# Kernel tuning notes

Hardware: AMD Instinct MI355X
Metric: run time of the kernel (lower is better)

## Reference

```python
import jax, jax.numpy as jnp
import numpy as np

D_INPUT = 900; D_MODEL = 900; D_STATE = 16; D_CONV = 4
D_INNER = 1800; DT_RANK = 57  # ceil(900/16)
B_SZ = 2; L = 900


def build_pe():
    # Faithful to the (non-standard) loop in PositionalEncoding.__init__
    pos = np.arange(D_INPUT, dtype=np.float64)[:, None]
    pe = np.zeros((D_INPUT, D_MODEL), dtype=np.float64)
    i_even = np.arange(0, D_MODEL, 2, dtype=np.float64)
    i_odd = np.arange(1, D_MODEL, 2, dtype=np.float64)
    pe[:, 0::2] = np.sin(pos / 10000.0 ** (2.0 * i_even / D_MODEL))
    pe[:, 1::2] = np.cos(pos / 10000.0 ** (2.0 * (i_odd + 1.0) / D_MODEL))
    return jnp.asarray(pe, jnp.float32)


def setup_inputs() -> dict:
    key = jax.random.key(0)
    ks = jax.random.split(key, 8)
    s = 0.02
    inp = jax.random.normal(ks[0], (B_SZ, L, D_INPUT), jnp.float32)
    W_emb = jax.random.normal(ks[1], (D_MODEL, D_INPUT), jnp.float32) * s
    b_emb = jnp.zeros((D_MODEL,), jnp.float32)
    norm_w = jnp.ones((D_MODEL,), jnp.float32)
    W_in = jax.random.normal(ks[2], (2 * D_INNER, D_MODEL), jnp.float32) * s
    conv_w = jax.random.normal(ks[3], (D_INNER, 1, D_CONV), jnp.float32) * s
    conv_b = jnp.zeros((D_INNER,), jnp.float32)
    W_xp = jax.random.normal(ks[4], (DT_RANK + 2 * D_STATE, D_INNER), jnp.float32) * s
    W_dt = jax.random.normal(ks[5], (D_INNER, DT_RANK), jnp.float32) * s
    b_dt = jnp.zeros((D_INNER,), jnp.float32)
    A_log = jnp.log(jnp.broadcast_to(jnp.arange(1, D_STATE + 1, dtype=jnp.float32), (D_INNER, D_STATE)))
    D = jnp.ones((D_INNER,), jnp.float32)
    W_out = jax.random.normal(ks[6], (D_MODEL, D_INNER), jnp.float32) * s
    normf_w = jnp.ones((D_MODEL,), jnp.float32)
    pe = build_pe()
    return dict(inp=inp, W_emb=W_emb, b_emb=b_emb, norm_w=norm_w, W_in=W_in,
                conv_w=conv_w, conv_b=conv_b, W_xp=W_xp, W_dt=W_dt, b_dt=b_dt,
                A_log=A_log, D=D, W_out=W_out, normf_w=normf_w, pe=pe)


def rmsnorm(x, w, eps=1e-5):
    return x * jax.lax.rsqrt(jnp.mean(x * x, axis=-1, keepdims=True) + eps) * w


def causal_dwconv(x, w, b):
    # x: (b, l, d_in); torch Conv1d(groups=d_in, padding=k-1) then [:, :, :l] == causal left-pad
    xc = jnp.transpose(x, (0, 2, 1))  # (b, d_in, l)
    y = jax.lax.conv_general_dilated(xc, w, window_strides=(1,),
                                     padding=[(D_CONV - 1, 0)],
                                     dimension_numbers=('NCH', 'OIH', 'NCH'),
                                     feature_group_count=D_INNER)
    return jnp.transpose(y + b[None, :, None], (0, 2, 1))


def selective_scan(u, delta, A, Bm, Cm, Dv):
    # u, delta: (b, l, d_in); A: (d_in, n); Bm, Cm: (b, l, n); Dv: (d_in,)
    dA = jnp.exp(jnp.einsum('bld,dn->bldn', delta, A))
    dBu = jnp.einsum('bld,bln,bld->bldn', delta, Bm, u)

    def step(h, xs):
        dA_i, dBu_i, C_i = xs
        h = dA_i * h + dBu_i                      # (b, d_in, n)
        y = jnp.einsum('bdn,bn->bd', h, C_i)
        return h, y

    h0 = jnp.zeros((u.shape[0], D_INNER, D_STATE), u.dtype)
    _, ys = jax.lax.scan(step, h0, (jnp.moveaxis(dA, 1, 0), jnp.moveaxis(dBu, 1, 0), jnp.moveaxis(Cm, 1, 0)))
    return jnp.moveaxis(ys, 0, 1) + u * Dv


def mamba_block(x, W_in, conv_w, conv_b, W_xp, W_dt, b_dt, A_log, Dv, W_out):
    xr = x @ W_in.T                               # (b, l, 2*d_inner)
    xm, res = xr[..., :D_INNER], xr[..., D_INNER:]
    xb = xm[..., ::-1]  # NOTE: original flips dim 2 == channel dim, not sequence
    xm = jax.nn.silu(causal_dwconv(xm, conv_w, conv_b))
    xb = jax.nn.silu(causal_dwconv(xb, conv_w, conv_b))

    def ssm(u):
        A = -jnp.exp(A_log)
        xd = u @ W_xp.T                           # (b, l, dt_rank + 2n)
        delta = jax.nn.softplus(xd[..., :DT_RANK] @ W_dt.T + b_dt)
        Bm = xd[..., DT_RANK:DT_RANK + D_STATE]
        Cm = xd[..., DT_RANK + D_STATE:]
        return selective_scan(u, delta, A, Bm, Cm, Dv)

    y = ssm(xm)
    yb = ssm(xb)[..., ::-1]  # flip back over channels, as in original
    g = jax.nn.silu(res)
    return (y * g + yb * g) @ W_out.T


def reference(inp, W_emb, b_emb, norm_w, W_in, conv_w, conv_b, W_xp, W_dt, b_dt, A_log, D, W_out, normf_w, pe):
    x = inp @ W_emb.T + b_emb                     # embedding Linear
    x = x * jnp.sqrt(jnp.float32(D_MODEL)) + pe[None, :x.shape[1]]
    x = mamba_block(rmsnorm(x, norm_w), W_in, conv_w, conv_b, W_xp, W_dt, b_dt, A_log, D, W_out) + x
    x = rmsnorm(x, normf_w)
    logits = x.reshape(x.shape[0], -1)
    return (logits,)
```

## Files before the change

### kernel.cpp

```cpp
#include <hip/hip_runtime.h>
#include <math.h>

typedef unsigned short ushortT;
typedef short short8 __attribute__((ext_vector_type(8)));
typedef float f32x4 __attribute__((ext_vector_type(4)));

#define D_STATE 16
#define D_INNER 1800
#define DT_RANK 57
#define SEQ_L 900
#define MROWS 1800
#define MP 1920
#define KP_DM 960
#define KP_DI 1856
#define KP_DT 64
#define NCHUNK 45
#define CLEN 20

__device__ __forceinline__ ushortT f2bf(float f) {
    unsigned u = __float_as_uint(f);
    unsigned r = (u + 0x7FFFu + ((u >> 16) & 1u)) >> 16;
    return (ushortT)r;
}
__device__ __forceinline__ float bf2f(ushortT h) {
    return __uint_as_float((unsigned)h << 16);
}
__device__ __forceinline__ float silu_f(float x) { return x / (1.f + __expf(-x)); }
__device__ __forceinline__ float softplus_f(float x) {
    return fmaxf(x, 0.f) + __logf(1.f + __expf(-fabsf(x)));
}

__device__ __forceinline__ void gload_lds16(const ushortT* g, ushortT* l) {
    __builtin_amdgcn_global_load_lds((const __attribute__((address_space(1))) unsigned int*)g,
                                     (__attribute__((address_space(3))) unsigned int*)l,
                                     16, 0, 0);
}

__global__ __launch_bounds__(256)
void cvt_all_k(const float* __restrict__ s0, ushortT* __restrict__ d0,
               const float* __restrict__ s1, ushortT* __restrict__ d1,
               const float* __restrict__ s2, ushortT* __restrict__ d2,
               const float* __restrict__ s3, ushortT* __restrict__ d3,
               const float* __restrict__ s4, ushortT* __restrict__ d4,
               const float* __restrict__ s5, ushortT* __restrict__ d5)
{
    const float* src; ushortT* dst; int M, K, Mp, Kp;
    switch (blockIdx.y) {
      case 0: src=s0; dst=d0; M=1800; K=900;  Mp=1920; Kp=960;  break;
      case 1: src=s1; dst=d1; M=900;  K=900;  Mp=1024; Kp=960;  break;
      case 2: src=s2; dst=d2; M=3600; K=900;  Mp=3712; Kp=960;  break;
      case 3: src=s3; dst=d3; M=89;   K=1800; Mp=128;  Kp=1856; break;
      case 4: src=s4; dst=d4; M=1800; K=57;   Mp=1920; Kp=64;   break;
      default:src=s5; dst=d5; M=900;  K=1800; Mp=1024; Kp=1856; break;
    }
    int t = blockIdx.x * 256 + threadIdx.x;
    int K4 = Kp >> 2;
    if (t >= Mp * K4) return;
    int r = t / K4, c4 = (t - r * K4) * 4;
    ushortT o[4];
#pragma unroll
    for (int e = 0; e < 4; ++e) {
        int c = c4 + e;
        float v = (r < M && c < K) ? src[(size_t)r * K + c] : 0.f;
        o[e] = f2bf(v);
    }
    uint2 pk;
    pk.x = (unsigned)o[0] | ((unsigned)o[1] << 16);
    pk.y = (unsigned)o[2] | ((unsigned)o[3] << 16);
    *(uint2*)(dst + (size_t)r * Kp + c4) = pk;
}

__global__ __launch_bounds__(256)
void gemm_mfma_k(const ushortT* __restrict__ A0, const ushortT* __restrict__ A1, int lda,
                 const ushortT* __restrict__ Bw, int ldb, int nkTotal, int split,
                 float* __restrict__ C0, float* __restrict__ C1, int ldc, size_t cstride,
                 ushortT* __restrict__ X0, ushortT* __restrict__ X1, int ldx, size_t xstride,
                 int M, int N, const float* __restrict__ bias, int mode)
{
    __shared__ ushortT As[2][128 * 64];
    __shared__ ushortT Bs[2][128 * 64];

    int gx = gridDim.x, gy = gridDim.y;
    int nwg = gx * gy * gridDim.z;
    int orig = (blockIdx.z * gy + blockIdx.y) * gx + blockIdx.x;
    int q8 = nwg >> 3, r8 = nwg & 7;
    int xcd = orig & 7, i8 = orig >> 3;
    int wg = (xcd < r8 ? xcd * (q8 + 1) : r8 * (q8 + 1) + (xcd - r8) * q8) + i8;
    int bx = wg % gx; int tmp = wg / gx; int by = tmp % gy; int bz = tmp / gy;

    int dir = bz / split, s = bz % split;
    int per = (nkTotal + split - 1) / split;
    int kt0 = s * per;
    int kcnt = nkTotal - kt0; if (kcnt > per) kcnt = per;
    int ktEnd = kt0 + kcnt;

    const ushortT* A = dir ? A1 : A0;
    float* C = (dir ? C1 : C0);
    ushortT* Xo = (dir ? X1 : X0);
    if (C)  C  += (size_t)s * cstride;
    if (Xo) Xo += (size_t)s * xstride;

    int tid = threadIdx.x;
    int lane = tid & 63, wave = tid >> 6;
    int wr = wave >> 1, wc = wave & 1;
    int m0 = by * 128, n0 = bx * 128;

    int csw = ((((tid >> 3) & 7) ^ (tid & 7)) << 3);
    auto stage = [&](int sb, int kt) {
#pragma unroll
        for (int r = 0; r < 4; ++r) {
            int idx = r * 256 + tid;
            int row = idx >> 3;
            gload_lds16(A + (size_t)(m0 + row) * lda + kt * 64 + csw, &As[sb][idx * 8]);
        }
#pragma unroll
        for (int r = 0; r < 4; ++r) {
            int idx = r * 256 + tid;
            int row = idx >> 3;
            gload_lds16(Bw + (size_t)(n0 + row) * ldb + kt * 64 + csw, &Bs[sb][idx * 8]);
        }
    };

    f32x4 acc[4][4] = {};
    int rmask = (lane & 7) << 3;

    stage(0, kt0);
    for (int t = kt0; t < ktEnd; ++t) {
        int cur = (t - kt0) & 1;
        if (t + 1 < ktEnd) {
            stage(cur ^ 1, t + 1);
            asm volatile("s_waitcnt vmcnt(8)" ::: "memory");
        } else {
            asm volatile("s_waitcnt vmcnt(0)" ::: "memory");
        }
        __builtin_amdgcn_s_barrier();
        __builtin_amdgcn_sched_barrier(0);
#pragma unroll
        for (int ks = 0; ks < 2; ++ks) {
            short8 av[4], bv[4];
            int kcol = (ks * 32 + (lane >> 4) * 8) ^ rmask;
#pragma unroll
            for (int i = 0; i < 4; ++i)
                av[i] = *(const short8*)(&As[cur][(wr * 64 + i * 16 + (lane & 15)) * 64 + kcol]);
#pragma unroll
            for (int j = 0; j < 4; ++j)
                bv[j] = *(const short8*)(&Bs[cur][(wc * 64 + j * 16 + (lane & 15)) * 64 + kcol]);
#pragma unroll
            for (int i = 0; i < 4; ++i)
#pragma unroll
                for (int j = 0; j < 4; ++j)
                    acc[i][j] = __builtin_amdgcn_mfma_f32_16x16x32_bf16(bv[j], av[i], acc[i][j], 0, 0, 0);
        }
        __builtin_amdgcn_sched_barrier(0);
        __builtin_amdgcn_s_barrier();
        __builtin_amdgcn_sched_barrier(0);
    }

#pragma unroll
    for (int i = 0; i < 4; ++i) {
        int m = m0 + wr * 64 + i * 16 + (lane & 15);
        if (m >= M) continue;
#pragma unroll
        for (int j = 0; j < 4; ++j) {
            int nb = n0 + wc * 64 + j * 16 + (lane >> 4) * 4;
            if (nb >= N) continue;
            f32x4 v = acc[i][j];
            if (mode == 5) {
#pragma unroll
                for (int e = 0; e < 4; ++e)
                    v[e] = softplus_f(v[e] + bias[nb + e]);
            }
            if (mode == 1 || mode == 5) {
                unsigned lo, hi;
                asm("v_cvt_pk_bf16_f32 %0, %1, %2" : "=v"(lo) : "v"(v[0]), "v"(v[1]));
                asm("v_cvt_pk_bf16_f32 %0, %1, %2" : "=v"(hi) : "v"(v[2]), "v"(v[3]));
                uint2 pk; pk.x = lo; pk.y = hi;
                *(uint2*)(Xo + (size_t)m * ldx + nb) = pk;
            } else {
                *(f32x4*)(C + (size_t)m * ldc + nb) = v;
            }
        }
    }
}

__global__ __launch_bounds__(256)
void rmsnorm_emb_k(const ushortT* __restrict__ P, size_t pstride,
                   const float* __restrict__ b_emb, const float* __restrict__ pe,
                   const float* __restrict__ norm_w,
                   float* __restrict__ XS, ushortT* __restrict__ XN, int ldxn)
{
    int row = blockIdx.x;
    int l = (row >= SEQ_L) ? row - SEQ_L : row;
    float vv[4];
    float ssum = 0.f;
#pragma unroll
    for (int k = 0; k < 4; ++k) {
        int c = threadIdx.x + k * 256;
        if (c < 900) {
            size_t i = (size_t)row * 900 + c;
            float a = bf2f(P[i]) + bf2f(P[i + pstride]) + bf2f(P[i + 2 * pstride]) + bf2f(P[i + 3 * pstride]);
            float v = 30.f * (a + b_emb[c]) + pe[(size_t)l * 900 + c];
            vv[k] = v;
            ssum += v * v;
        } else vv[k] = 0.f;
    }
#pragma unroll
    for (int off = 32; off; off >>= 1) ssum += __shfl_down(ssum, off, 64);
    __shared__ float red[4];
    int wv = threadIdx.x >> 6;
    if ((threadIdx.x & 63) == 0) red[wv] = ssum;
    __syncthreads();
    float tot = red[0] + red[1] + red[2] + red[3];
    float scale = rsqrtf(tot / 900.f + 1e-5f);
#pragma unroll
    for (int k = 0; k < 4; ++k) {
        int c = threadIdx.x + k * 256;
        if (c < 900) {
            XS[(size_t)row * 900 + c] = vv[k];
            XN[(size_t)row * ldxn + c] = f2bf(vv[k] * scale * norm_w[c]);
        }
    }
}

__global__ __launch_bounds__(256)
void rmsnorm_final_k(const ushortT* __restrict__ ZP, size_t zstride,
                     const float* __restrict__ XS, const float* __restrict__ w,
                     float* __restrict__ out)
{
    int row = blockIdx.x;
    float vv[4];
    float ssum = 0.f;
#pragma unroll
    for (int k = 0; k < 4; ++k) {
        int c = threadIdx.x + k * 256;
        if (c < 900) {
            size_t i = (size_t)row * 900 + c;
            float v = bf2f(ZP[i]) + bf2f(ZP[i + zstride]) + bf2f(ZP[i + 2 * zstride]) + bf2f(ZP[i + 3 * zstride]) + XS[i];
            vv[k] = v;
            ssum += v * v;
        } else vv[k] = 0.f;
    }
#pragma unroll
    for (int off = 32; off; off >>= 1) ssum += __shfl_down(ssum, off, 64);
    __shared__ float red[4];
    int wv = threadIdx.x >> 6;
    if ((threadIdx.x & 63) == 0) red[wv] = ssum;
    __syncthreads();
    float tot = red[0] + red[1] + red[2] + red[3];
    float scale = rsqrtf(tot / 900.f + 1e-5f);
#pragma unroll
    for (int k = 0; k < 4; ++k) {
        int c = threadIdx.x + k * 256;
        if (c < 900) out[(size_t)row * 900 + c] = vv[k] * scale * w[c];
    }
}

__global__ __launch_bounds__(256)
void conv_silu_k(const ushortT* __restrict__ xr0, const ushortT* __restrict__ xr1,
                 const float* __restrict__ w, const float* __restrict__ cb,
                 ushortT* __restrict__ xmc, ushortT* __restrict__ xbc,
                 ushortT* __restrict__ gout)
{
    int t = blockIdx.x * 256 + threadIdx.x;
    if (t >= MROWS * (D_INNER / 2)) return;
    int d0 = (t % (D_INNER / 2)) * 2;
    int row = t / (D_INNER / 2);
    int l = row % SEQ_L;
    float w0[4], w1[4];
#pragma unroll
    for (int k = 0; k < 4; ++k) { w0[k] = w[d0 * 4 + k]; w1[k] = w[d0 * 4 + 4 + k]; }
    int rdp = 1798 - d0;
    float sf0 = cb[d0], sf1 = cb[d0 + 1];
    float sb0 = sf0, sb1 = sf1;
#pragma unroll
    for (int k = 0; k < 4; ++k) {
        int ll = l - 3 + k;
        if (ll < 0) continue;
        size_t ro = (size_t)(row - l + ll) * 3600;
        unsigned f0 = *(const unsigned*)(xr0 + ro + d0);
        unsigned f1 = *(const unsigned*)(xr1 + ro + d0);
        float a0 = bf2f((ushortT)f0) + bf2f((ushortT)f1);
        float a1 = bf2f((ushortT)(f0 >> 16)) + bf2f((ushortT)(f1 >> 16));
        sf0 = fmaf(w0[k], a0, sf0);
        sf1 = fmaf(w1[k], a1, sf1);
        unsigned r0 = *(const unsigned*)(xr0 + ro + rdp);
        unsigned r1 = *(const unsigned*)(xr1 + ro + rdp);
        float b0 = bf2f((ushortT)(r0 >> 16)) + bf2f((ushortT)(r1 >> 16));
        float b1 = bf2f((ushortT)r0) + bf2f((ushortT)r1);
        sb0 = fmaf(w0[k], b0, sb0);
        sb1 = fmaf(w1[k], b1, sb1);
    }
    unsigned om = (unsigned)f2bf(silu_f(sf0)) | ((unsigned)f2bf(silu_f(sf1)) << 16);
    unsigned ob = (unsigned)f2bf(silu_f(sb0)) | ((unsigned)f2bf(silu_f(sb1)) << 16);
    *(unsigned*)(xmc + (size_t)row * KP_DI + d0) = om;
    *(unsigned*)(xbc + (size_t)row * KP_DI + d0) = ob;
    size_t rr = (size_t)row * 3600 + D_INNER + d0;
    unsigned g0 = *(const unsigned*)(xr0 + rr);
    unsigned g1 = *(const unsigned*)(xr1 + rr);
    float ga = silu_f(bf2f((ushortT)g0) + bf2f((ushortT)g1));
    float gb = silu_f(bf2f((ushortT)(g0 >> 16)) + bf2f((ushortT)(g1 >> 16)));
    *(unsigned*)(gout + (size_t)row * D_INNER + d0) = (unsigned)f2bf(ga) | ((unsigned)f2bf(gb) << 16);
}

__global__ __launch_bounds__(256)
void xp_reduce_k(const float* __restrict__ XPp, size_t pstride,
                 float* __restrict__ XDC, ushortT* __restrict__ XDMb, ushortT* __restrict__ XDBb)
{
    int t = blockIdx.x * 256 + threadIdx.x;
    if (t >= 2 * MROWS * 96) return;
    int dir = t / (MROWS * 96);
    int rem = t - dir * (MROWS * 96);
    int row = rem / 96, c = rem - row * 96;
    const float* basep = XPp + (size_t)dir * 8 * pstride + (size_t)row * 96 + c;
    float s = 0.f;
#pragma unroll
    for (int p = 0; p < 8; ++p) s += basep[p * pstride];
    ushortT* xdb = dir ? XDBb : XDMb;
    if (c < DT_RANK)           xdb[(size_t)row * KP_DT + c] = f2bf(s);
    else if (c < KP_DT)        xdb[(size_t)row * KP_DT + c] = 0;
    if (c >= DT_RANK && c < DT_RANK + 2 * D_STATE)
        XDC[((size_t)dir * MROWS + row) * 32 + (c - DT_RANK)] = s;
}

__global__ __launch_bounds__(256)
void scan_l1_k(const ushortT* __restrict__ DMb, const ushortT* __restrict__ DBb,
               const ushortT* __restrict__ Um, const ushortT* __restrict__ Ub,
               const float* __restrict__ XDC, const float* __restrict__ A_log,
               ushortT* __restrict__ HL, float* __restrict__ SD)
{
    int d = blockIdx.x * 256 + threadIdx.x;
    if (d >= D_INNER) return;
    int c = blockIdx.y, zz = blockIdx.z;
    int b = zz >> 1, dir = zz & 1;
    const ushortT* DL = dir ? DBb : DMb;
    const ushortT* U = dir ? Ub : Um;
    const float* XD = XDC + (size_t)dir * MROWS * 32;
    float Aa[D_STATE];
#pragma unroll
    for (int n = 0; n < D_STATE; ++n) Aa[n] = -__expf(A_log[d * D_STATE + n]);
    float h[D_STATE] = {};
    float S = 0.f;
    int l0 = c * CLEN;
    for (int i = 0; i < CLEN; ++i) {
        size_t rowi = (size_t)b * SEQ_L + l0 + i;
        float delta = bf2f(DL[rowi * D_INNER + d]);
        float u = bf2f(U[rowi * KP_DI + d]);
        const float* bc = XD + rowi * 32;
        float du = delta * u;
        S += delta;
#pragma unroll
        for (int n = 0; n < D_STATE; ++n)
            h[n] = fmaf(__expf(delta * Aa[n]), h[n], du * bc[n]);
    }
    ushortT* hp = HL + ((size_t)(zz * NCHUNK + c) * D_INNER + d) * D_STATE;
    unsigned pk[8];
#pragma unroll
    for (int q = 0; q < 8; ++q)
        asm("v_cvt_pk_bf16_f32 %0, %1, %2" : "=v"(pk[q]) : "v"(h[2*q]), "v"(h[2*q+1]));
    uint4 lo4; lo4.x = pk[0]; lo4.y = pk[1]; lo4.z = pk[2]; lo4.w = pk[3];
    uint4 hi4; hi4.x = pk[4]; hi4.y = pk[5]; hi4.z = pk[6]; hi4.w = pk[7];
    *(uint4*)(hp) = lo4;
    *(uint4*)(hp + 8) = hi4;
    SD[(size_t)(zz * NCHUNK + c) * D_INNER + d] = S;
}

__global__ __launch_bounds__(256)
void scan_l2_k(ushortT* __restrict__ HL, const float* __restrict__ SD,
               const float* __restrict__ A_log)
{
    int t = blockIdx.x * 256 + threadIdx.x;
    if (t >= 4 * D_INNER * D_STATE) return;
    int n = t & 15;
    int d = (t >> 4) % D_INNER;
    int zz = t / (D_INNER * D_STATE);
    float Aa = -__expf(A_log[d * D_STATE + n]);
    float h0 = 0.f;
    for (int c = 0; c < NCHUNK; ++c) {
        size_t ih = ((size_t)(zz * NCHUNK + c) * D_INNER + d) * D_STATE + n;
        float hl = bf2f(HL[ih]);
        float T = __expf(Aa * SD[(size_t)(zz * NCHUNK + c) * D_INNER + d]);
        HL[ih] = f2bf(h0);
        h0 = fmaf(T, h0, hl);
    }
}

__global__ __launch_bounds__(256)
void scan3_gate_k(const ushortT* __restrict__ DMb, const ushortT* __restrict__ DBb,
                  const ushortT* __restrict__ Um, const ushortT* __restrict__ Ub,
                  const float* __restrict__ XDC, const float* __restrict__ A_log,
                  const float* __restrict__ Dv, const ushortT* __restrict__ HL,
                  const ushortT* __restrict__ G, ushortT* __restrict__ YC)
{
    int d = blockIdx.x * 256 + threadIdx.x;
    if (d >= D_INNER) return;
    int c = blockIdx.y, b = blockIdx.z;
    int rd = D_INNER - 1 - d;
    float Aa0[D_STATE], Aa1[D_STATE], h0[D_STATE], h1[D_STATE];
#pragma unroll
    for (int n = 0; n < D_STATE; ++n) Aa0[n] = -__expf(A_log[d * D_STATE + n]);
#pragma unroll
    for (int n = 0; n < D_STATE; ++n) Aa1[n] = -__expf(A_log[rd * D_STATE + n]);
    const ushortT* hp0 = HL + ((size_t)((b * 2) * NCHUNK + c) * D_INNER + d) * D_STATE;
    const ushortT* hp1 = HL + ((size_t)((b * 2 + 1) * NCHUNK + c) * D_INNER + rd) * D_STATE;
    {
        uint4 a0 = *(const uint4*)(hp0);
        uint4 a1 = *(const uint4*)(hp0 + 8);
        unsigned ww[8] = {a0.x, a0.y, a0.z, a0.w, a1.x, a1.y, a1.z, a1.w};
#pragma unroll
        for (int q = 0; q < 8; ++q) {
            h0[2*q]   = bf2f((ushortT)ww[q]);
            h0[2*q+1] = bf2f((ushortT)(ww[q] >> 16));
        }
        uint4 b0 = *(const uint4*)(hp1);
        uint4 b1 = *(const uint4*)(hp1 + 8);
        unsigned vv[8] = {b0.x, b0.y, b0.z, b0.w, b1.x, b1.y, b1.z, b1.w};
#pragma unroll
        for (int q = 0; q < 8; ++q) {
            h1[2*q]   = bf2f((ushortT)vv[q]);
            h1[2*q+1] = bf2f((ushortT)(vv[q] >> 16));
        }
    }
    float Dd0 = Dv[d], Dd1 = Dv[rd];
    const float* XD0 = XDC;
    const float* XD1 = XDC + (size_t)MROWS * 32;
    int l0 = c * CLEN;
    for (int i = 0; i < CLEN; ++i) {
        size_t rowi = (size_t)b * SEQ_L + l0 + i;
        float delta0 = bf2f(DMb[rowi * D_INNER + d]);
        float u0 = bf2f(Um[rowi * KP_DI + d]);
        const float* bc0 = XD0 + rowi * 32;
        float du0 = delta0 * u0;
        float acc0 = u0 * Dd0;
#pragma unroll
        for (int n = 0; n < D_STATE; ++n) {
            h0[n] = fmaf(__expf(delta0 * Aa0[n]), h0[n], du0 * bc0[n]);
            acc0 = fmaf(h0[n], bc0[D_STATE + n], acc0);
        }
        float delta1 = bf2f(DBb[rowi * D_INNER + rd]);
        float u1 = bf2f(Ub[rowi * KP_DI + rd]);
        const float* bc1 = XD1 + rowi * 32;
        float du1 = delta1 * u1;
        float acc1 = u1 * Dd1;
#pragma unroll
        for (int n = 0; n < D_STATE; ++n) {
            h1[n] = fmaf(__expf(delta1 * Aa1[n]), h1[n], du1 * bc1[n]);
            acc1 = fmaf(h1[n], bc1[D_STATE + n], acc1);
        }
        float g = bf2f(G[rowi * D_INNER + d]);
        YC[rowi * KP_DI + d] = f2bf((acc0 + acc1) * g);
    }
}

extern "C" void kernel_launch(void* const* d_in, const int* in_sizes, int n_in,
                              void* d_out, int out_size, void* d_ws, size_t ws_size,
                              hipStream_t stream)
{
    const float* inp    = (const float*)d_in[0];
    const float* W_emb  = (const float*)d_in[1];
    const float* b_emb  = (const float*)d_in[2];
    const float* norm_w = (const float*)d_in[3];
    const float* W_in   = (const float*)d_in[4];
    const float* conv_w = (const float*)d_in[5];
    const float* conv_b = (const float*)d_in[6];
    const float* W_xp   = (const float*)d_in[7];
    const float* W_dt   = (const float*)d_in[8];
    const float* b_dt   = (const float*)d_in[9];
    const float* A_log  = (const float*)d_in[10];
    const float* Dv     = (const float*)d_in[11];
    const float* W_out  = (const float*)d_in[12];
    const float* normf_w= (const float*)d_in[13];
    const float* pe     = (const float*)d_in[14];

    char* base = (char*)d_ws;
    size_t off = 0;
    auto alloc = [&](size_t bytes) { char* p = base + off; off += (bytes + 255) & ~(size_t)255; return p; };

    float*   XS      = (float*)alloc(6480000);
    char*    arena1  = alloc(22032000);
    float*   XPp     = (float*)arena1;
    ushortT* HL      = (ushortT*)arena1;
    float*   SD      = (float*)(arena1 + 10368000);
    ushortT* inp_bf  = (ushortT*)alloc(3686400);
    ushortT* XN_bf   = (ushortT*)alloc(3686400);
    ushortT* Wemb_bf = (ushortT*)alloc(1966080);
    ushortT* Win_bf  = (ushortT*)alloc(7127040);
    ushortT* Wxp_bf  = (ushortT*)alloc(475136);
    ushortT* Wdt_bf  = (ushortT*)alloc(245760);
    ushortT* Wout_bf = (ushortT*)alloc(3801088);
    ushortT* XBC_bf  = (ushortT*)alloc(7127040);
    char*    arena2  = alloc(25920000);
    ushortT* Pemb    = (ushortT*)arena2;
    ushortT* XR0     = (ushortT*)arena2;
    ushortT* XR1     = XR0 + (size_t)MROWS * 3600;
    ushortT* DMb     = (ushortT*)arena2;
    ushortT* DBb     = DMb + (size_t)MROWS * D_INNER;
    ushortT* ZP      = (ushortT*)arena2;
    ushortT* G_bf    = (ushortT*)alloc(6480000);

    float*   XDC     = (float*)Wemb_bf;
    ushortT* XDM_bf  = (ushortT*)((char*)Wemb_bf + 460800);
    ushortT* XDB_bf  = (ushortT*)((char*)Wemb_bf + 706560);
    ushortT* XMC_bf  = Win_bf;
    ushortT* YC_bf   = inp_bf;

    dim3 blk(256);
    auto cdiv = [](int a, int b) { return (a + b - 1) / b; };
    const size_t PSTR  = 1620000;
    const size_t XPSTR = 172800;
    const size_t XRSTR = (size_t)MROWS * 3600;

    hipLaunchKernelGGL(cvt_all_k, dim3(3480, 6), blk, 0, stream,
                       inp, inp_bf, W_emb, Wemb_bf, W_in, Win_bf,
                       W_xp, Wxp_bf, W_dt, Wdt_bf, W_out, Wout_bf);
    hipLaunchKernelGGL(gemm_mfma_k, dim3(8, 15, 4), blk, 0, stream,
                       inp_bf, inp_bf, KP_DM, Wemb_bf, KP_DM, KP_DM/64, 4,
                       (float*)nullptr, (float*)nullptr, 0, (size_t)0,
                       Pemb, Pemb, 900, PSTR,
                       MROWS, 900, (const float*)nullptr, 1);
    hipLaunchKernelGGL(rmsnorm_emb_k, dim3(MROWS), blk, 0, stream,
                       Pemb, PSTR, b_emb, pe, norm_w, XS, XN_bf, KP_DM);
    hipLaunchKernelGGL(gemm_mfma_k, dim3(29, 15, 2), blk, 0, stream,
                       XN_bf, XN_bf, KP_DM, Win_bf, KP_DM, KP_DM/64, 2,
                       (float*)nullptr, (float*)nullptr, 0, (size_t)0,
                       XR0, XR0, 3600, XRSTR,
                       MROWS, 3600, (const float*)nullptr, 1);
    hipLaunchKernelGGL(conv_silu_k, dim3(cdiv(MROWS * (D_INNER/2), 256)), blk, 0, stream,
                       XR0, XR1, conv_w, conv_b, XMC_bf, XBC_bf, G_bf);
    hipLaunchKernelGGL(gemm_mfma_k, dim3(1, 15, 16), blk, 0, stream,
                       XMC_bf, XBC_bf, KP_DI, Wxp_bf, KP_DI, KP_DI/64, 8,
                       XPp, XPp + 8 * XPSTR, 96, XPSTR,
                       (ushortT*)nullptr, (ushortT*)nullptr, 0, (size_t)0,
                       MROWS, 96, (const float*)nullptr, 0);
    hipLaunchKernelGGL(xp_reduce_k, dim3(cdiv(2 * MROWS * 96, 256)), blk, 0, stream,
                       XPp, XPSTR, XDC, XDM_bf, XDB_bf);
    hipLaunchKernelGGL(gemm_mfma_k, dim3(15, 15, 2), blk, 0, stream,
                       XDM_bf, XDB_bf, KP_DT, Wdt_bf, KP_DT, 1, 1,
                       (float*)nullptr, (float*)nullptr, 0, (size_t)0,
                       DMb, DBb, D_INNER, (size_t)0,
                       MROWS, D_INNER, b_dt, 5);
    hipLaunchKernelGGL(scan_l1_k, dim3(cdiv(D_INNER, 256), NCHUNK, 4), blk, 0, stream,
                       DMb, DBb, XMC_bf, XBC_bf, XDC, A_log, HL, SD);
    hipLaunchKernelGGL(scan_l2_k, dim3(cdiv(4 * D_INNER * D_STATE, 256)), blk, 0, stream, HL, SD, A_log);
    hipLaunchKernelGGL(scan3_gate_k, dim3(cdiv(D_INNER, 256), NCHUNK, 2), blk, 0, stream,
                       DMb, DBb, XMC_bf, XBC_bf, XDC, A_log, Dv, HL, G_bf, YC_bf);
    hipLaunchKernelGGL(gemm_mfma_k, dim3(8, 15, 4), blk, 0, stream,
                       YC_bf, YC_bf, KP_DI, Wout_bf, KP_DI, KP_DI/64, 4,
                       (float*)nullptr, (float*)nullptr, 0, (size_t)0,
                       ZP, ZP, 900, PSTR,
                       MROWS, 900, (const float*)nullptr, 1);
    hipLaunchKernelGGL(rmsnorm_final_k, dim3(MROWS), blk, 0, stream,
                       ZP, PSTR, XS, normf_w, (float*)d_out);
}
```

Measured before the change: 284.7 us.

## Drop split-K on in_proj GEMM, fuse gate SiLU into epilogue, widen conv/cvt vectors

Measured after the change: 276.7 us. 1.03x faster.

```diff
diff --git a/kernel.cpp b/kernel.cpp
--- a/kernel.cpp
+++ b/kernel.cpp
@@ -54,20 +54,19 @@
       default:src=s5; dst=d5; M=900;  K=1800; Mp=1024; Kp=1856; break;
     }
     int t = blockIdx.x * 256 + threadIdx.x;
-    int K4 = Kp >> 2;
-    if (t >= Mp * K4) return;
-    int r = t / K4, c4 = (t - r * K4) * 4;
-    ushortT o[4];
-#pragma unroll
-    for (int e = 0; e < 4; ++e) {
-        int c = c4 + e;
-        float v = (r < M && c < K) ? src[(size_t)r * K + c] : 0.f;
-        o[e] = f2bf(v);
-    }
-    uint2 pk;
-    pk.x = (unsigned)o[0] | ((unsigned)o[1] << 16);
-    pk.y = (unsigned)o[2] | ((unsigned)o[3] << 16);
-    *(uint2*)(dst + (size_t)r * Kp + c4) = pk;
+    int K8 = Kp >> 3;
+    if (t >= Mp * K8) return;
+    int r = t / K8, c8 = (t - r * K8) * 8;
+    unsigned pk[4];
+#pragma unroll
+    for (int q = 0; q < 4; ++q) {
+        int ca = c8 + 2 * q, cb = ca + 1;
+        float va = (r < M && ca < K) ? src[(size_t)r * K + ca] : 0.f;
+        float vb = (r < M && cb < K) ? src[(size_t)r * K + cb] : 0.f;
+        pk[q] = (unsigned)f2bf(va) | ((unsigned)f2bf(vb) << 16);
+    }
+    uint4 o; o.x = pk[0]; o.y = pk[1]; o.z = pk[2]; o.w = pk[3];
+    *(uint4*)(dst + (size_t)r * Kp + c8) = o;
 }
 
 __global__ __launch_bounds__(256)
@@ -97,7 +96,7 @@
     const ushortT* A = dir ? A1 : A0;
     float* C = (dir ? C1 : C0);
     ushortT* Xo = (dir ? X1 : X0);
-    if (C)  C  += (size_t)s * cstride;
+    if (C && mode != 6)  C  += (size_t)s * cstride;
     if (Xo) Xo += (size_t)s * xstride;
 
     int tid = threadIdx.x;
@@ -170,7 +169,24 @@
                 for (int e = 0; e < 4; ++e)
                     v[e] = softplus_f(v[e] + bias[nb + e]);
             }
-            if (mode == 1 || mode == 5) {
+            if (mode == 6) {
+                if (nb < D_INNER) {
+                    unsigned lo, hi;
+                    asm("v_cvt_pk_bf16_f32 %0, %1, %2" : "=v"(lo) : "v"(v[0]), "v"(v[1]));
+                    asm("v_cvt_pk_bf16_f32 %0, %1, %2" : "=v"(hi) : "v"(v[2]), "v"(v[3]));
+                    uint2 pk; pk.x = lo; pk.y = hi;
+                    *(uint2*)(Xo + (size_t)m * ldx + nb) = pk;
+                } else {
+                    ushortT* G = (ushortT*)C;
+#pragma unroll
+                    for (int e = 0; e < 4; ++e) v[e] = silu_f(v[e]);
+                    unsigned lo, hi;
+                    asm("v_cvt_pk_bf16_f32 %0, %1, %2" : "=v"(lo) : "v"(v[0]), "v"(v[1]));
+                    asm("v_cvt_pk_bf16_f32 %0, %1, %2" : "=v"(hi) : "v"(v[2]), "v"(v[3]));
+                    uint2 pk; pk.x = lo; pk.y = hi;
+                    *(uint2*)(G + (size_t)m * D_INNER + (nb - D_INNER)) = pk;
+                }
+            } else if (mode == 1 || mode == 5) {
                 unsigned lo, hi;
                 asm("v_cvt_pk_bf16_f32 %0, %1, %2" : "=v"(lo) : "v"(v[0]), "v"(v[1]));
                 asm("v_cvt_pk_bf16_f32 %0, %1, %2" : "=v"(hi) : "v"(v[2]), "v"(v[3]));
@@ -256,50 +272,51 @@
 }
 
 __global__ __launch_bounds__(256)
-void conv_silu_k(const ushortT* __restrict__ xr0, const ushortT* __restrict__ xr1,
+void conv_silu_k(const ushortT* __restrict__ xr,
                  const float* __restrict__ w, const float* __restrict__ cb,
-                 ushortT* __restrict__ xmc, ushortT* __restrict__ xbc,
-                 ushortT* __restrict__ gout)
+                 ushortT* __restrict__ xmc, ushortT* __restrict__ xbc)
 {
     int t = blockIdx.x * 256 + threadIdx.x;
-    if (t >= MROWS * (D_INNER / 2)) return;
-    int d0 = (t % (D_INNER / 2)) * 2;
-    int row = t / (D_INNER / 2);
+    if (t >= MROWS * (D_INNER / 4)) return;
+    int d0 = (t % (D_INNER / 4)) * 4;
+    int row = t / (D_INNER / 4);
     int l = row % SEQ_L;
-    float w0[4], w1[4];
-#pragma unroll
-    for (int k = 0; k < 4; ++k) { w0[k] = w[d0 * 4 + k]; w1[k] = w[d0 * 4 + 4 + k]; }
-    int rdp = 1798 - d0;
-    float sf0 = cb[d0], sf1 = cb[d0 + 1];
-    float sb0 = sf0, sb1 = sf1;
+    float wv[4][4], sf[4], sb[4];
+#pragma unroll
+    for (int ch = 0; ch < 4; ++ch) {
+        f32x4 wl = *(const f32x4*)(w + (d0 + ch) * 4);
+        wv[ch][0] = wl[0]; wv[ch][1] = wl[1]; wv[ch][2] = wl[2]; wv[ch][3] = wl[3];
+        float b = cb[d0 + ch];
+        sf[ch] = b; sb[ch] = b;
+    }
+    int rdp = 1796 - d0;
 #pragma unroll
     for (int k = 0; k < 4; ++k) {
         int ll = l - 3 + k;
         if (ll < 0) continue;
-        size_t ro = (size_t)(row - l + ll) * 3600;
-        unsigned f0 = *(const unsigned*)(xr0 + ro + d0);
-        unsigned f1 = *(const unsigned*)(xr1 + ro + d0);
-        float a0 = bf2f((ushortT)f0) + bf2f((ushortT)f1);
-        float a1 = bf2f((ushortT)(f0 >> 16)) + bf2f((ushortT)(f1 >> 16));
-        sf0 = fmaf(w0[k], a0, sf0);
-        sf1 = fmaf(w1[k], a1, sf1);
-        unsigned r0 = *(const unsigned*)(xr0 + ro + rdp);
-        unsigned r1 = *(const unsigned*)(xr1 + ro + rdp);
-        float b0 = bf2f((ushortT)(r0 >> 16)) + bf2f((ushortT)(r1 >> 16));
-        float b1 = bf2f((ushortT)r0) + bf2f((ushortT)r1);
-        sb0 = fmaf(w0[k], b0, sb0);
-        sb1 = fmaf(w1[k], b1, sb1);
-    }
-    unsigned om = (unsigned)f2bf(silu_f(sf0)) | ((unsigned)f2bf(silu_f(sf1)) << 16);
-    unsigned ob = (unsigned)f2bf(silu_f(sb0)) | ((unsigned)f2bf(silu_f(sb1)) << 16);
-    *(unsigned*)(xmc + (size_t)row * KP_DI + d0) = om;
-    *(unsigned*)(xbc + (size_t)row * KP_DI + d0) = ob;
-    size_t rr = (size_t)row * 3600 + D_INNER + d0;
-    unsigned g0 = *(const unsigned*)(xr0 + rr);
-    unsigned g1 = *(const unsigned*)(xr1 + rr);
-    float ga = silu_f(bf2f((ushortT)g0) + bf2f((ushortT)g1));
-    float gb = silu_f(bf2f((ushortT)(g0 >> 16)) + bf2f((ushortT)(g1 >> 16)));
-    *(unsigned*)(gout + (size_t)row * D_INNER + d0) = (unsigned)f2bf(ga) | ((unsigned)f2bf(gb) << 16);
+        const ushortT* rp = xr + (size_t)(row - l + ll) * D_INNER;
+        uint2 f = *(const uint2*)(rp + d0);
+        float a0 = bf2f((ushortT)f.x), a1 = bf2f((ushortT)(f.x >> 16));
+        float a2 = bf2f((ushortT)f.y), a3 = bf2f((ushortT)(f.y >> 16));
+        sf[0] = fmaf(wv[0][k], a0, sf[0]);
+        sf[1] = fmaf(wv[1][k], a1, sf[1]);
+        sf[2] = fmaf(wv[2][k], a2, sf[2]);
+        sf[3] = fmaf(wv[3][k], a3, sf[3]);
+        uint2 rv = *(const uint2*)(rp + rdp);
+        float b0 = bf2f((ushortT)rv.x), b1 = bf2f((ushortT)(rv.x >> 16));
+        float b2 = bf2f((ushortT)rv.y), b3 = bf2f((ushortT)(rv.y >> 16));
+        sb[0] = fmaf(wv[0][k], b3, sb[0]);
+        sb[1] = fmaf(wv[1][k], b2, sb[1]);
+        sb[2] = fmaf(wv[2][k], b1, sb[2]);
+        sb[3] = fmaf(wv[3][k], b0, sb[3]);
+    }
+    uint2 om, ob;
+    om.x = (unsigned)f2bf(silu_f(sf[0])) | ((unsigned)f2bf(silu_f(sf[1])) << 16);
+    om.y = (unsigned)f2bf(silu_f(sf[2])) | ((unsigned)f2bf(silu_f(sf[3])) << 16);
+    ob.x = (unsigned)f2bf(silu_f(sb[0])) | ((unsigned)f2bf(silu_f(sb[1])) << 16);
+    ob.y = (unsigned)f2bf(silu_f(sb[2])) | ((unsigned)f2bf(silu_f(sb[3])) << 16);
+    *(uint2*)(xmc + (size_t)row * KP_DI + d0) = om;
+    *(uint2*)(xbc + (size_t)row * KP_DI + d0) = ob;
 }
 
 __global__ __launch_bounds__(256)
@@ -490,8 +507,7 @@
     ushortT* XBC_bf  = (ushortT*)alloc(7127040);
     char*    arena2  = alloc(25920000);
     ushortT* Pemb    = (ushortT*)arena2;
-    ushortT* XR0     = (ushortT*)arena2;
-    ushortT* XR1     = XR0 + (size_t)MROWS * 3600;
+    ushortT* XR      = (ushortT*)arena2;
     ushortT* DMb     = (ushortT*)arena2;
     ushortT* DBb     = DMb + (size_t)MROWS * D_INNER;
     ushortT* ZP      = (ushortT*)arena2;
@@ -507,9 +523,8 @@
     auto cdiv = [](int a, int b) { return (a + b - 1) / b; };
     const size_t PSTR  = 1620000;
     const size_t XPSTR = 172800;
-    const size_t XRSTR = (size_t)MROWS * 3600;
-
-    hipLaunchKernelGGL(cvt_all_k, dim3(3480, 6), blk, 0, stream,
+
+    hipLaunchKernelGGL(cvt_all_k, dim3(1740, 6), blk, 0, stream,
                        inp, inp_bf, W_emb, Wemb_bf, W_in, Win_bf,
                        W_xp, Wxp_bf, W_dt, Wdt_bf, W_out, Wout_bf);
     hipLaunchKernelGGL(gemm_mfma_k, dim3(8, 15, 4), blk, 0, stream,
@@ -519,13 +534,13 @@
                        MROWS, 900, (const float*)nullptr, 1);
     hipLaunchKernelGGL(rmsnorm_emb_k, dim3(MROWS), blk, 0, stream,
                        Pemb, PSTR, b_emb, pe, norm_w, XS, XN_bf, KP_DM);
-    hipLaunchKernelGGL(gemm_mfma_k, dim3(29, 15, 2), blk, 0, stream,
-                       XN_bf, XN_bf, KP_DM, Win_bf, KP_DM, KP_DM/64, 2,
-                       (float*)nullptr, (float*)nullptr, 0, (size_t)0,
-                       XR0, XR0, 3600, XRSTR,
-                       MROWS, 3600, (const float*)nullptr, 1);
-    hipLaunchKernelGGL(conv_silu_k, dim3(cdiv(MROWS * (D_INNER/2), 256)), blk, 0, stream,
-                       XR0, XR1, conv_w, conv_b, XMC_bf, XBC_bf, G_bf);
+    hipLaunchKernelGGL(gemm_mfma_k, dim3(29, 15, 1), blk, 0, stream,
+                       XN_bf, XN_bf, KP_DM, Win_bf, KP_DM, KP_DM/64, 1,
+                       (float*)G_bf, (float*)G_bf, 0, (size_t)0,
+                       XR, XR, D_INNER, (size_t)0,
+                       MROWS, 3600, (const float*)nullptr, 6);
+    hipLaunchKernelGGL(conv_silu_k, dim3(cdiv(MROWS * (D_INNER/4), 256)), blk, 0, stream,
+                       XR, conv_w, conv_b, XMC_bf, XBC_bf);
     hipLaunchKernelGGL(gemm_mfma_k, dim3(1, 15, 16), blk, 0, stream,
                        XMC_bf, XBC_bf, KP_DI, Wxp_bf, KP_DI, KP_DI/64, 8,
                        XPp, XPp + 8 * XPSTR, 96, XPSTR,
```
